# Kernel optimization log

Measured on AMD Instinct MI355X. Metric: run time of the kernel, lower is better.

The kernel has to match this reference:

```python
import jax, jax.numpy as jnp
import numpy as np
from jax import lax

P_COARSE, P_FINE = 8, 4
EMBED_DIM = 128


def _patchify(x, p):
    # torch unfold(kernel=p, stride=p) then transpose: [B, Hp*Wp, C*p*p]
    B, C, H, W = x.shape
    Hp, Wp = H // p, W // p
    t = x.reshape(B, C, Hp, p, Wp, p).transpose(0, 2, 4, 1, 3, 5)
    return t.reshape(B, Hp * Wp, C * p * p), Hp, Wp


def _edge_map(x):
    gray = x.mean(axis=1, keepdims=True)
    kx = jnp.array([[-1., 0., 1.], [-2., 0., 2.], [-1., 0., 1.]], gray.dtype)[None, None]
    ky = jnp.array([[-1., -2., -1.], [0., 0., 0.], [1., 2., 1.]], gray.dtype)[None, None]
    pad = [(1, 1), (1, 1)]
    sx = lax.conv_general_dilated(gray, kx, (1, 1), pad)
    sy = lax.conv_general_dilated(gray, ky, (1, 1), pad)
    e = jnp.sqrt(sx * sx + sy * sy)
    B, _, H, W = e.shape
    # avg_pool2d(4, stride=4)
    return e.reshape(B, 1, H // 4, 4, W // 4, 4).mean(axis=(3, 5))


def _compact(tok, m):
    # stream-compact masked rows to the front, zero-pad the rest (pad_sequence semantics, padded to full Nf)
    Nf, D = tok.shape
    pos = jnp.cumsum(m) - 1
    pos = jnp.where(m, pos, Nf)  # unmasked rows go to overflow slot
    out = jnp.zeros((Nf + 1, D), tok.dtype).at[pos].set(tok)
    return out[:Nf]


def setup_inputs() -> dict:
    key = jax.random.key(0)
    ks = jax.random.split(key, 6)
    D = EMBED_DIM
    pd_c = 1 * P_COARSE * P_COARSE
    pd_f = 1 * P_FINE * P_FINE
    return {
        "x": jax.random.normal(ks[0], (8, 1, 512, 512), jnp.float32),
        "w_coarse": jax.random.normal(ks[1], (pd_c, D), jnp.float32) / np.sqrt(pd_c),
        "b_coarse": jnp.zeros((D,), jnp.float32),
        "w_fine": jax.random.normal(ks[2], (pd_f, D), jnp.float32) / np.sqrt(pd_f),
        "b_fine": jnp.zeros((D,), jnp.float32),
        "type_emb": jax.random.normal(ks[3], (2, D), jnp.float32) * 0.02,
    }


def reference(x, w_coarse, b_coarse, w_fine, b_fine, type_emb):
    B = x.shape[0]
    # coarse branch
    pc, Hc, Wc = _patchify(x, P_COARSE)
    coarse = pc @ w_coarse + b_coarse + type_emb[0]  # [B, Nc, D]
    # edge-driven mask
    edges = _edge_map(x)  # [B,1,He,We]
    mask = edges > edges.mean(axis=(2, 3), keepdims=True)
    # fine branch
    pf, Hf, Wf = _patchify(x, P_FINE)
    fine = pf @ w_fine + b_fine  # [B, Nf, D]
    # nearest upsample mask to (Hf, Wf): integer factor repeat
    m = mask[:, 0]
    m = jnp.repeat(jnp.repeat(m, Hf // m.shape[1], axis=1), Wf // m.shape[2], axis=2)
    mask_flat = m.reshape(B, -1)  # [B, Nf]
    fine_c = jax.vmap(_compact)(fine, mask_flat) + type_emb[1]
    tokens = jnp.concatenate([coarse, fine_c], axis=1)
    return tokens, mask_flat
```

## Files before the change

kernel.cpp:

```cpp
#include <hip/hip_runtime.h>

#define IMH 512
#define IMW 512
#define BATCH 8
#define NTOK 20480
#define NC 4096
#define NF 16384
#define ED 128

typedef float vf4 __attribute__((ext_vector_type(4)));
typedef int   vi4 __attribute__((ext_vector_type(4)));

__device__ __forceinline__ void nt_store4(float* p, float a, float b, float c, float d) {
    vf4 v = {a, b, c, d};
    __builtin_nontemporal_store(v, (vf4*)p);
}
__device__ __forceinline__ void nt_store4v(float* p, float4 v) {
    nt_store4(p, v.x, v.y, v.z, v.w);
}

__global__ __launch_bounds__(256) void fused_edge_coarse(const float* __restrict__ x,
                                                         const float* __restrict__ wc,
                                                         const float* __restrict__ bc,
                                                         const float* __restrict__ temb,
                                                         float* __restrict__ out,
                                                         double* __restrict__ edges) {
    __shared__ union {
        float esm[66][68];
        float smc[8][128];
    } U;
    int blk = blockIdx.x;
    int t = threadIdx.x;
    if (blk < 2048) {
        int b = blk >> 8;
        int p0 = (blk & 255) * 16;
        int hp = p0 >> 6;
        int wp0 = p0 & 63;
        int d = t & 127;
        int h = t >> 7;
        float wcol[64];
        #pragma unroll
        for (int k = 0; k < 64; ++k) wcol[k] = wc[k * ED + d];
        const float* img = x + ((size_t)b * IMH + hp * 8) * IMW + wp0 * 8;
        {
            int r = t >> 5, c4 = t & 31;
            *(float4*)&U.smc[r][c4 * 4] = *(const float4*)&img[r * IMW + c4 * 4];
        }
        __syncthreads();
        float base = bc[d] + temb[d];
        float* dst = out + ((size_t)b * NTOK + p0 + h * 8) * ED + d;
        #pragma unroll
        for (int p = 0; p < 8; ++p) {
            int col0 = h * 64 + p * 8;
            float acc = base;
            #pragma unroll
            for (int r = 0; r < 8; ++r) {
                float4 v0 = *(const float4*)&U.smc[r][col0];
                float4 v1 = *(const float4*)&U.smc[r][col0 + 4];
                acc += v0.x * wcol[r * 8 + 0] + v0.y * wcol[r * 8 + 1]
                     + v0.z * wcol[r * 8 + 2] + v0.w * wcol[r * 8 + 3]
                     + v1.x * wcol[r * 8 + 4] + v1.y * wcol[r * 8 + 5]
                     + v1.z * wcol[r * 8 + 6] + v1.w * wcol[r * 8 + 7];
            }
            __builtin_nontemporal_store(acc, dst + (size_t)p * ED);
        }
    } else {
        int blk2 = blk - 2048;
        int b = blk2 >> 6;
        int tile = blk2 & 63;
        int ty0 = (tile >> 3) * 64;
        int tx0 = (tile & 7) * 64;
        const float* img = x + (size_t)b * (IMH * IMW);
        for (int idx = t; idx < 66 * 66; idx += 256) {
            int r = idx / 66, c = idx - r * 66;
            int gy = ty0 - 1 + r, gx = tx0 - 1 + c;
            float v = 0.f;
            if (gy >= 0 && gy < IMH && gx >= 0 && gx < IMW) v = img[gy * IMW + gx];
            U.esm[r][c] = v;
        }
        __syncthreads();
        int cy = t >> 4, cx = t & 15;
        double acc = 0.0;
        #pragma unroll
        for (int dy = 0; dy < 4; ++dy) {
            int py = cy * 4 + dy + 1;
            #pragma unroll
            for (int dx = 0; dx < 4; ++dx) {
                int px = cx * 4 + dx + 1;
                double a00 = (double)U.esm[py - 1][px - 1];
                double a01 = (double)U.esm[py - 1][px];
                double a02 = (double)U.esm[py - 1][px + 1];
                double a10 = (double)U.esm[py][px - 1];
                double a12 = (double)U.esm[py][px + 1];
                double a20 = (double)U.esm[py + 1][px - 1];
                double a21 = (double)U.esm[py + 1][px];
                double a22 = (double)U.esm[py + 1][px + 1];
                double sx = (a02 + 2.0 * a12 + a22) - (a00 + 2.0 * a10 + a20);
                double sy = (a20 + 2.0 * a21 + a22) - (a00 + 2.0 * a01 + a02);
                acc += sqrt(sx * sx + sy * sy);
            }
        }
        int gy = (ty0 >> 2) + cy;
        int gx = (tx0 >> 2) + cx;
        edges[((size_t)b << 14) + gy * 128 + gx] = acc * (1.0 / 16.0);
    }
}

__global__ __launch_bounds__(1024) void scan_kernel(const double* __restrict__ edges,
                                                    int* __restrict__ pos,
                                                    int* __restrict__ Karr,
                                                    float* __restrict__ mask_out) {
    int b = blockIdx.x;
    const double* e = edges + ((size_t)b << 14);
    int t = threadIdx.x;
    int lane = t & 63, wid = t >> 6;
    double v[16];
    #pragma unroll
    for (int j = 0; j < 8; ++j) {
        double2 dv = *(const double2*)&e[t * 16 + j * 2];
        v[2 * j] = dv.x; v[2 * j + 1] = dv.y;
    }
    double s = 0.0;
    #pragma unroll
    for (int j = 0; j < 16; ++j) s += v[j];
    #pragma unroll
    for (int off = 32; off > 0; off >>= 1) s += __shfl_xor(s, off);
    __shared__ double wsum[16];
    __shared__ int wcnt[16];
    if (lane == 0) wsum[wid] = s;
    __syncthreads();
    double total = 0.0;
    #pragma unroll
    for (int w = 0; w < 16; ++w) total += wsum[w];
    double mean = total * (1.0 / 16384.0);
    int m[16], cnt = 0;
    #pragma unroll
    for (int j = 0; j < 16; ++j) { m[j] = (v[j] > mean) ? 1 : 0; cnt += m[j]; }
    int incl = cnt;
    #pragma unroll
    for (int off = 1; off < 64; off <<= 1) {
        int up = __shfl_up(incl, off);
        if (lane >= off) incl += up;
    }
    if (lane == 63) wcnt[wid] = incl;
    __syncthreads();
    int woff = 0, Ktot = 0;
    #pragma unroll
    for (int w = 0; w < 16; ++w) { int c = wcnt[w]; Ktot += c; if (w < wid) woff += c; }
    int run = woff + incl - cnt;
    float mf[16]; int pv[16];
    #pragma unroll
    for (int j = 0; j < 16; ++j) {
        pv[j] = m[j] ? run : -1;
        run += m[j];
        mf[j] = m[j] ? 1.0f : 0.0f;
    }
    float* mb = mask_out + ((size_t)b << 14) + t * 16;
    int* pb = pos + ((size_t)b << 14) + t * 16;
    #pragma unroll
    for (int q = 0; q < 4; ++q) {
        nt_store4(&mb[q * 4], mf[4 * q], mf[4 * q + 1], mf[4 * q + 2], mf[4 * q + 3]);
        *(int4*)&pb[q * 4] = make_int4(pv[4 * q], pv[4 * q + 1], pv[4 * q + 2], pv[4 * q + 3]);
    }
    if (t == 0) Karr[b] = Ktot;
}

__global__ __launch_bounds__(256) void fine_kernel(const float* __restrict__ x,
                                                   const float* __restrict__ wfp,
                                                   const float* __restrict__ bfp,
                                                   const float* __restrict__ temb,
                                                   const int* __restrict__ pos,
                                                   const int* __restrict__ Karr,
                                                   float* __restrict__ out) {
    int b = blockIdx.y;
    int i0 = blockIdx.x * 64;
    int hf = i0 >> 7;
    int wf0 = i0 & 127;
    int t = threadIdx.x;
    int d4 = t & 31;
    int g = t >> 5;
    __shared__ float smx[4][256];
    float4 wcol[16];
    #pragma unroll
    for (int k = 0; k < 16; ++k) wcol[k] = *(const float4*)&wfp[k * ED + d4 * 4];
    const float* img = x + ((size_t)b * IMH + hf * 4) * IMW + wf0 * 4;
    {
        int r = t >> 6, c4 = t & 63;
        *(float4*)&smx[r][c4 * 4] = *(const float4*)&img[r * IMW + c4 * 4];
    }
    __syncthreads();
    int K = Karr[b];
    const int* posb = pos + ((size_t)b << 14);
    float4 fill = *(const float4*)&temb[ED + d4 * 4];
    float4 bse = *(const float4*)&bfp[d4 * 4];
    float4 base = make_float4(bse.x + fill.x, bse.y + fill.y, bse.z + fill.z, bse.w + fill.w);
    float* tok = out + ((size_t)b * NTOK + NC) * ED;
    #pragma unroll
    for (int pp = 0; pp < 8; ++pp) {
        int p = g + pp * 8;
        int i = i0 + p;
        int ps = posb[i];
        if (ps >= 0) {
            float4 acc = base;
            #pragma unroll
            for (int r = 0; r < 4; ++r) {
                float4 vv = *(const float4*)&smx[r][p * 4];
                acc.x += vv.x * wcol[4 * r].x + vv.y * wcol[4 * r + 1].x + vv.z * wcol[4 * r + 2].x + vv.w * wcol[4 * r + 3].x;
                acc.y += vv.x * wcol[4 * r].y + vv.y * wcol[4 * r + 1].y + vv.z * wcol[4 * r + 2].y + vv.w * wcol[4 * r + 3].y;
                acc.z += vv.x * wcol[4 * r].z + vv.y * wcol[4 * r + 1].z + vv.z * wcol[4 * r + 2].z + vv.w * wcol[4 * r + 3].z;
                acc.w += vv.x * wcol[4 * r].w + vv.y * wcol[4 * r + 1].w + vv.z * wcol[4 * r + 2].w + vv.w * wcol[4 * r + 3].w;
            }
            nt_store4v(tok + ((size_t)ps * 32 + d4) * 4, acc);
        }
        if (i >= K) {
            nt_store4v(tok + ((size_t)i * 32 + d4) * 4, fill);
        }
    }
}

extern "C" void kernel_launch(void* const* d_in, const int* in_sizes, int n_in,
                              void* d_out, int out_size, void* d_ws, size_t ws_size,
                              hipStream_t stream) {
    const float* x    = (const float*)d_in[0];
    const float* wc   = (const float*)d_in[1];
    const float* bc   = (const float*)d_in[2];
    const float* wfp  = (const float*)d_in[3];
    const float* bfp  = (const float*)d_in[4];
    const float* temb = (const float*)d_in[5];
    float* out = (float*)d_out;

    double* edges = (double*)d_ws;
    int* pos  = (int*)((char*)d_ws + (size_t)BATCH * NF * sizeof(double));
    int* Karr = (int*)((char*)d_ws + (size_t)BATCH * NF * (sizeof(double) + sizeof(int)));

    float* mask_out = out + (size_t)BATCH * NTOK * ED;

    fused_edge_coarse<<<dim3(2560), 256, 0, stream>>>(x, wc, bc, temb, out, edges);
    scan_kernel<<<dim3(BATCH), 1024, 0, stream>>>(edges, pos, Karr, mask_out);
    fine_kernel<<<dim3(256, BATCH), 256, 0, stream>>>(x, wfp, bfp, temb, pos, Karr, out);
}
```

Measured before the change: 53.33 us.

## Read coarse patches directly from global memory and double patches per block

The coarse-branch blocks no longer stage the 8x512 image strip in shared memory with a barrier. Each wavefront now covers 16 patches for half of the embedding columns, loading pixel values directly through wave-uniform (scalar) global loads, and each block handles 32 patches instead of 16. This removes LDS traffic and the __syncthreads, and halves the coarse block count so each block amortizes its weight-column register load over more patches. The trade-offs are more global/scalar load instructions per wave and fewer blocks to hide latency.

New measurement: 49.23 us. -7.7%, faster.

```diff
diff --git a/kernel.cpp b/kernel.cpp
--- a/kernel.cpp
+++ b/kernel.cpp
@@ -9,7 +9,6 @@
 #define ED 128
 
 typedef float vf4 __attribute__((ext_vector_type(4)));
-typedef int   vi4 __attribute__((ext_vector_type(4)));
 
 __device__ __forceinline__ void nt_store4(float* p, float a, float b, float c, float d) {
     vf4 v = {a, b, c, d};
@@ -25,47 +24,39 @@
                                                          const float* __restrict__ temb,
                                                          float* __restrict__ out,
                                                          double* __restrict__ edges) {
-    __shared__ union {
-        float esm[66][68];
-        float smc[8][128];
-    } U;
+    __shared__ float esm[66][68];
     int blk = blockIdx.x;
     int t = threadIdx.x;
-    if (blk < 2048) {
-        int b = blk >> 8;
-        int p0 = (blk & 255) * 16;
-        int hp = p0 >> 6;
-        int wp0 = p0 & 63;
-        int d = t & 127;
-        int h = t >> 7;
+    if (blk < 1024) {
+        int b = blk >> 7;
+        int pblk = (blk & 127) * 32;
+        int wv = __builtin_amdgcn_readfirstlane(t >> 6);
+        int lane = t & 63;
+        int h = wv & 1;
+        int p0 = pblk + (wv >> 1) * 16;
+        int d = h * 64 + lane;
         float wcol[64];
         #pragma unroll
         for (int k = 0; k < 64; ++k) wcol[k] = wc[k * ED + d];
-        const float* img = x + ((size_t)b * IMH + hp * 8) * IMW + wp0 * 8;
-        {
-            int r = t >> 5, c4 = t & 31;
-            *(float4*)&U.smc[r][c4 * 4] = *(const float4*)&img[r * IMW + c4 * 4];
-        }
-        __syncthreads();
         float base = bc[d] + temb[d];
-        float* dst = out + ((size_t)b * NTOK + p0 + h * 8) * ED + d;
+        const float* img = x + ((size_t)b * IMH + (p0 >> 6) * 8) * IMW + (p0 & 63) * 8;
+        float* dst = out + ((size_t)b * NTOK + p0) * ED + d;
         #pragma unroll
-        for (int p = 0; p < 8; ++p) {
-            int col0 = h * 64 + p * 8;
+        for (int p = 0; p < 16; ++p) {
+            const float* pimg = img + p * 8;
             float acc = base;
             #pragma unroll
             for (int r = 0; r < 8; ++r) {
-                float4 v0 = *(const float4*)&U.smc[r][col0];
-                float4 v1 = *(const float4*)&U.smc[r][col0 + 4];
-                acc += v0.x * wcol[r * 8 + 0] + v0.y * wcol[r * 8 + 1]
-                     + v0.z * wcol[r * 8 + 2] + v0.w * wcol[r * 8 + 3]
-                     + v1.x * wcol[r * 8 + 4] + v1.y * wcol[r * 8 + 5]
-                     + v1.z * wcol[r * 8 + 6] + v1.w * wcol[r * 8 + 7];
+                const float* rp = pimg + r * IMW;
+                acc += rp[0] * wcol[r * 8 + 0] + rp[1] * wcol[r * 8 + 1]
+                     + rp[2] * wcol[r * 8 + 2] + rp[3] * wcol[r * 8 + 3]
+                     + rp[4] * wcol[r * 8 + 4] + rp[5] * wcol[r * 8 + 5]
+                     + rp[6] * wcol[r * 8 + 6] + rp[7] * wcol[r * 8 + 7];
             }
             __builtin_nontemporal_store(acc, dst + (size_t)p * ED);
         }
     } else {
-        int blk2 = blk - 2048;
+        int blk2 = blk - 1024;
         int b = blk2 >> 6;
         int tile = blk2 & 63;
         int ty0 = (tile >> 3) * 64;
@@ -76,7 +67,7 @@
             int gy = ty0 - 1 + r, gx = tx0 - 1 + c;
             float v = 0.f;
             if (gy >= 0 && gy < IMH && gx >= 0 && gx < IMW) v = img[gy * IMW + gx];
-            U.esm[r][c] = v;
+            esm[r][c] = v;
         }
         __syncthreads();
         int cy = t >> 4, cx = t & 15;
@@ -87,14 +78,14 @@
             #pragma unroll
             for (int dx = 0; dx < 4; ++dx) {
                 int px = cx * 4 + dx + 1;
-                double a00 = (double)U.esm[py - 1][px - 1];
-                double a01 = (double)U.esm[py - 1][px];
-                double a02 = (double)U.esm[py - 1][px + 1];
-                double a10 = (double)U.esm[py][px - 1];
-                double a12 = (double)U.esm[py][px + 1];
-                double a20 = (double)U.esm[py + 1][px - 1];
-                double a21 = (double)U.esm[py + 1][px];
-                double a22 = (double)U.esm[py + 1][px + 1];
+                double a00 = (double)esm[py - 1][px - 1];
+                double a01 = (double)esm[py - 1][px];
+                double a02 = (double)esm[py - 1][px + 1];
+                double a10 = (double)esm[py][px - 1];
+                double a12 = (double)esm[py][px + 1];
+                double a20 = (double)esm[py + 1][px - 1];
+                double a21 = (double)esm[py + 1][px];
+                double a22 = (double)esm[py + 1][px + 1];
                 double sx = (a02 + 2.0 * a12 + a22) - (a00 + 2.0 * a10 + a20);
                 double sy = (a20 + 2.0 * a21 + a22) - (a00 + 2.0 * a01 + a02);
                 acc += sqrt(sx * sx + sy * sy);
@@ -235,7 +226,7 @@
 
     float* mask_out = out + (size_t)BATCH * NTOK * ED;
 
-    fused_edge_coarse<<<dim3(2560), 256, 0, stream>>>(x, wc, bc, temb, out, edges);
+    fused_edge_coarse<<<dim3(1536), 256, 0, stream>>>(x, wc, bc, temb, out, edges);
     scan_kernel<<<dim3(BATCH), 1024, 0, stream>>>(edges, pos, Karr, mask_out);
     fine_kernel<<<dim3(256, BATCH), 256, 0, stream>>>(x, wfp, bfp, temb, pos, Karr, out);
 }
```
